# Optimization experiments

Measured on AMD Instinct MI355X. Metric: run time of the kernel, lower is better.

The kernel has to match this reference:

```python
import jax, jax.numpy as jnp
import numpy as np

D_MODEL = 1024
N_HEADS = 16
D_HEAD = D_MODEL // N_HEADS


def setup_inputs() -> dict:
    key = jax.random.key(0)
    k1, k2, k3 = jax.random.split(key, 3)
    x = jax.random.normal(k1, (2, 2048, D_MODEL), dtype=jnp.float32)
    # torch Linear weights transposed to [in, out] for x @ W
    w_qkv = jax.random.normal(k2, (D_MODEL, 3 * D_MODEL), dtype=jnp.float32) * (D_MODEL ** -0.5)
    w_proj = jax.random.normal(k3, (D_MODEL, D_MODEL), dtype=jnp.float32) * (D_MODEL ** -0.5)
    return {"x": x, "w_qkv": w_qkv, "w_proj": w_proj}


def reference(x, w_qkv, w_proj):
    B, N, D = x.shape
    qkv = x @ w_qkv                              # [B, N, 3D]
    q, k, v = jnp.split(qkv, 3, axis=-1)         # each [B, N, D]

    def split_heads(t):
        return t.reshape(B, N, N_HEADS, D_HEAD).transpose(0, 2, 1, 3)  # [B, H, N, d]

    q, k, v = map(split_heads, (q, k, v))
    scale = 1.0 / jnp.sqrt(jnp.float32(D_HEAD))
    scores = jnp.einsum('bhnd,bhmd->bhnm', q, k) * scale   # [B, H, N, N]
    attn = jax.nn.softmax(scores, axis=-1)
    out = jnp.einsum('bhnm,bhmd->bhnd', attn, v)            # [B, H, N, d]
    out = out.transpose(0, 2, 1, 3).reshape(B, N, D)        # merge heads
    return out @ w_proj + x
```

## Files before the change

### kernel.cpp

```cpp
#include <hip/hip_runtime.h>
#include <hip/hip_bf16.h>
#include <cstdint>
#include <cstddef>

typedef __bf16 bf16;
typedef __attribute__((ext_vector_type(4))) float f32x4;
typedef __attribute__((ext_vector_type(16))) float f32x16;
typedef __attribute__((ext_vector_type(8))) __bf16 bf16x8;
typedef __attribute__((ext_vector_type(4))) __bf16 bf16x4;
typedef __attribute__((ext_vector_type(4))) unsigned int u32x4;

#define D_MODEL 1024
#define NHEADS  16
#define DHEAD   64
#define SEQ     2048
#define BATCH   2
#define MROWS   (BATCH*SEQ)
#define BHTOT   (BATCH*NHEADS)

#define QSCALE 0.18033688011112042f
#define DEFER_THR 11.5f

__device__ __forceinline__ void gload16(const bf16* g, bf16* l) {
  __builtin_amdgcn_global_load_lds(
      (const __attribute__((address_space(1))) void*)g,
      (__attribute__((address_space(3))) void*)l, 16, 0, 0);
}

__device__ __forceinline__ f32x4 mfma16(bf16x8 a, bf16x8 b, f32x4 c) {
  return __builtin_amdgcn_mfma_f32_16x16x32_bf16(a, b, c, 0, 0, 0);
}

__device__ __forceinline__ f32x16 mfma32(bf16x8 a, bf16x8 b, f32x16 c) {
  return __builtin_amdgcn_mfma_f32_32x32x16_bf16(a, b, c, 0, 0, 0);
}

__device__ __forceinline__ float fexp2(float x) {
#if __has_builtin(__builtin_amdgcn_exp2f)
  return __builtin_amdgcn_exp2f(x);
#else
  float r; asm("v_exp_f32 %0, %1" : "=v"(r) : "v"(x)); return r;
#endif
}

__device__ __forceinline__ unsigned cvtpk(float lo, float hi) {
  unsigned r;
  asm("v_cvt_pk_bf16_f32 %0, %1, %2" : "=v"(r) : "v"(lo), "v"(hi));
  return r;
}


__global__ void cast_f32_bf16(const float* __restrict__ in, bf16* __restrict__ out, int n4) {
  int i = blockIdx.x * blockDim.x + threadIdx.x;
  if (i >= n4) return;
  float4 v = ((const float4*)in)[i];
  bf16x4 o;
  o[0] = (bf16)v.x; o[1] = (bf16)v.y; o[2] = (bf16)v.z; o[3] = (bf16)v.w;
  ((bf16x4*)out)[i] = o;
}

__global__ void tcast(const float* __restrict__ in, bf16* __restrict__ out, int R, int C) {
  __shared__ float t[32][33];
  int c0 = blockIdx.x * 32, r0 = blockIdx.y * 32;
  int tx = threadIdx.x, ty = threadIdx.y;
  #pragma unroll
  for (int i = 0; i < 4; i++)
    t[ty + i*8][tx] = in[(size_t)(r0 + ty + i*8) * C + c0 + tx];
  __syncthreads();
  #pragma unroll
  for (int i = 0; i < 4; i++)
    out[(size_t)(c0 + ty + i*8) * R + r0 + tx] = (bf16)t[tx][ty + i*8];
}


template <int EPI>
__global__ __launch_bounds__(256, 3) void gemm_bt(
    const bf16* __restrict__ A, const bf16* __restrict__ Bt, int K, int N,
    bf16* __restrict__ qb, bf16* __restrict__ kb, bf16* __restrict__ vtb,
    const float* __restrict__ xres, float* __restrict__ outf) {
  __shared__ alignas(16) bf16 As[128 * 64];
  __shared__ alignas(16) bf16 Bs[128 * 64];
  const int tid = threadIdx.x;
  const int wave = tid >> 6, lane = tid & 63;
  const int wr = wave >> 1, wc = wave & 1;
  const int m0 = blockIdx.y * 128, n0 = blockIdx.x * 128;
  const int srow = lane >> 3;
  const int scol = ((lane & 7) ^ srow) * 8;
  const int lr16 = lane & 15, lg = lane >> 4;
  const int rsw = (lr16 & 7) << 4;
  const int cA = (lg * 16) ^ rsw;
  const int cB = (64 + lg * 16) ^ rsw;
  const char* aP = (const char*)As + (wr*64 + lr16) * 128;
  const char* bP = (const char*)Bs + (wc*64 + lr16) * 128;

  f32x4 acc[4][4];
  #pragma unroll
  for (int m = 0; m < 4; m++)
    #pragma unroll
    for (int n = 0; n < 4; n++) acc[m][n] = (f32x4)0.0f;

  for (int k0 = 0; k0 < K; k0 += 64) {
    #pragma unroll
    for (int j = 0; j < 4; j++) {
      const int c = wave * 4 + j;
      gload16(A  + (size_t)(m0 + c*8 + srow) * K + k0 + scol, &As[c * 512]);
      gload16(Bt + (size_t)(n0 + c*8 + srow) * K + k0 + scol, &Bs[c * 512]);
    }
    __syncthreads();
    bf16x8 af[4][2], bfr[4][2];
    #pragma unroll
    for (int m = 0; m < 4; m++) {
      af[m][0] = *(const bf16x8*)(aP + m*2048 + cA);
      af[m][1] = *(const bf16x8*)(aP + m*2048 + cB);
    }
    #pragma unroll
    for (int n = 0; n < 4; n++) {
      bfr[n][0] = *(const bf16x8*)(bP + n*2048 + cA);
      bfr[n][1] = *(const bf16x8*)(bP + n*2048 + cB);
    }
    #pragma unroll
    for (int m = 0; m < 4; m++)
      #pragma unroll
      for (int n = 0; n < 4; n++) {
        acc[m][n] = mfma16(af[m][0], bfr[n][0], acc[m][n]);
        acc[m][n] = mfma16(af[m][1], bfr[n][1], acc[m][n]);
      }
    __syncthreads();
  }

  #pragma unroll
  for (int n = 0; n < 4; n++) {
    const int colg = n0 + wc*64 + n*16 + lr16;
    if (EPI == 0) {
      const int which = colg >> 10;
      const int win = colg & 1023;
      const int h = win >> 6, d = win & 63;
      #pragma unroll
      for (int m = 0; m < 4; m++) {
        const int rowg0 = m0 + wr*64 + m*16 + lg*4;
        #pragma unroll
        for (int j = 0; j < 4; j++) {
          const int rowg = rowg0 + j;
          const int b = rowg >> 11, r = rowg & 2047;
          const int bh = (b << 4) + h;
          if (which == 2) {
            vtb[((size_t)bh * DHEAD + d) * SEQ + r] = (bf16)acc[m][n][j];
          } else {
            bf16* dst = (which == 0) ? qb : kb;
            const float sc = (which == 0) ? QSCALE : 1.0f;
            dst[((size_t)bh * SEQ + r) * DHEAD + d] = (bf16)(acc[m][n][j] * sc);
          }
        }
      }
    } else {
      #pragma unroll
      for (int m = 0; m < 4; m++) {
        const int rowg0 = m0 + wr*64 + m*16 + lg*4;
        #pragma unroll
        for (int j = 0; j < 4; j++) {
          const size_t idx = (size_t)(rowg0 + j) * N + colg;
          outf[idx] = acc[m][n][j] + xres[idx];
        }
      }
    }
  }
}

__global__ __launch_bounds__(512, 2) void attn_kernel(
    const bf16* __restrict__ q, const bf16* __restrict__ k,
    const bf16* __restrict__ vt, bf16* __restrict__ o) {
  __shared__ alignas(16) char smraw[65536];
  bf16* kvb = (bf16*)smraw;
  float* mg = (float*)smraw;

  const int tid = threadIdx.x;
  const int wave = tid >> 6, lane = tid & 63;
  const int qw = wave & 3, kh2 = wave >> 2;
  const int l31 = lane & 31, hi = lane >> 5;
  const int bh = blockIdx.y;
  const int b = bh >> 4, h = bh & 15;
  const int qr = blockIdx.x * 128 + qw * 32;
  const bf16* kh = k  + (size_t)bh * SEQ * DHEAD;
  const bf16* vh = vt + (size_t)bh * DHEAD * SEQ;

  const int srow = lane >> 3;
  const int scol = ((lane & 7) ^ srow) * 8;
  const bf16* kg = kh + (size_t)(kh2 * 1024 + qw * 16 + srow) * DHEAD + scol;
  const bf16* vg = vh + (size_t)(qw * 16 + srow) * SEQ + kh2 * 1024 + scol;
  bf16* ldsK0 = kvb + kh2 * 16384 +        qw * 1024;
  bf16* ldsK1 = kvb + kh2 * 16384 + 8192 + qw * 1024;
  bf16* ldsV0 = kvb + kh2 * 16384 + 4096 +        qw * 1024;
  bf16* ldsV1 = kvb + kh2 * 16384 + 8192 + 4096 + qw * 1024;

  const bf16* qrow = q + (size_t)bh * SEQ * DHEAD + (size_t)(qr + l31) * DHEAD;
  bf16x8 qf[4];
  #pragma unroll
  for (int ks = 0; ks < 4; ks++)
    qf[ks] = *(const bf16x8*)&qrow[ks * 16 + hi * 8];

  float mr = 0.0f, lsum = 0.0f;
  f32x16 acc0 = (f32x16)0.0f, acc1 = (f32x16)0.0f;

  const int rsw = (lane & 7) << 4;
  const int rowoff = l31 * 128;
  int cofs[4];
  #pragma unroll
  for (int ks = 0; ks < 4; ks++) cofs[ks] = (ks * 32 + hi * 16) ^ rsw;
  const char* kr0 = (const char*)(kvb + kh2 * 16384) + rowoff;
  const char* kr1 = (const char*)(kvb + kh2 * 16384 + 8192) + rowoff;
  const char* vr0 = (const char*)(kvb + kh2 * 16384 + 4096) + rowoff;
  const char* vr1 = (const char*)(kvb + kh2 * 16384 + 8192 + 4096) + rowoff;

  gload16(kg, ldsK0); gload16(kg + 8 * DHEAD, ldsK0 + 512);
  gload16(vg, ldsV0); gload16(vg + 8 * SEQ,   ldsV0 + 512);
  kg += 64 * DHEAD; vg += 64;
  __syncthreads();

  const int NT = 1024 / 64;
  for (int t = 0; t < NT; ++t) {
    bf16* dK = (t & 1) ? ldsK0 : ldsK1;
    bf16* dV = (t & 1) ? ldsV0 : ldsV1;
    if (t + 1 < NT) {
      gload16(kg, dK); gload16(kg + 8 * DHEAD, dK + 512);
      gload16(vg, dV); gload16(vg + 8 * SEQ,   dV + 512);
      kg += 64 * DHEAD; vg += 64;
    }
    const char* kr = (t & 1) ? kr1 : kr0;
    const char* vr = (t & 1) ? vr1 : vr0;

    #pragma unroll
    for (int th = 0; th < 2; ++th) {
      const int toff = th * 4096;

      const float nmr = -mr;
      f32x16 s = (f32x16)nmr;
      __builtin_amdgcn_s_setprio(1);
      #pragma unroll
      for (int ks = 0; ks < 4; ks++) {
        bf16x8 kf = *(const bf16x8*)(kr + toff + cofs[ks]);
        s = mfma32(kf, qf[ks], s);
      }
      __builtin_amdgcn_s_setprio(0);

      const float a0 = fmaxf(fmaxf(s[0], s[1]), fmaxf(s[2], s[3]));
      const float a1 = fmaxf(fmaxf(s[4], s[5]), fmaxf(s[6], s[7]));
      const float a2 = fmaxf(fmaxf(s[8], s[9]), fmaxf(s[10], s[11]));
      const float a3 = fmaxf(fmaxf(s[12], s[13]), fmaxf(s[14], s[15]));
      const float lmax = fmaxf(fmaxf(a0, a1), fmaxf(a2, a3));

      if (!__all(lmax <= DEFER_THR)) {
        float mx = fmaxf(lmax, __shfl_xor(lmax, 32));
        mx = fmaxf(mx, 0.0f);
        const float corr = fexp2(-mx);
        lsum *= corr;
        acc0 *= corr; acc1 *= corr;
        mr += mx;
        #pragma unroll
        for (int r = 0; r < 16; r++) s[r] -= mx;
      }

      #pragma unroll
      for (int r = 0; r < 16; r++) s[r] = fexp2(s[r]);
      lsum += (((s[0] + s[1]) + (s[2] + s[3])) + ((s[4] + s[5]) + (s[6] + s[7])))
            + (((s[8] + s[9]) + (s[10] + s[11])) + ((s[12] + s[13]) + (s[14] + s[15])));

      __builtin_amdgcn_s_setprio(1);
      #pragma unroll
      for (int u = 0; u < 2; ++u) {
        const unsigned w0 = cvtpk(s[8*u + 0], s[8*u + 1]);
        const unsigned w1 = cvtpk(s[8*u + 2], s[8*u + 3]);
        const unsigned w2 = cvtpk(s[8*u + 4], s[8*u + 5]);
        const unsigned w3 = cvtpk(s[8*u + 6], s[8*u + 7]);
        const unsigned p0 = (unsigned)__shfl_xor((int)w0, 32);
        const unsigned p1 = (unsigned)__shfl_xor((int)w1, 32);
        const unsigned p2 = (unsigned)__shfl_xor((int)w2, 32);
        const unsigned p3 = (unsigned)__shfl_xor((int)w3, 32);
        u32x4 fw;
        fw[0] = hi ? p2 : w0;
        fw[1] = hi ? p3 : w1;
        fw[2] = hi ? w2 : p0;
        fw[3] = hi ? w3 : p1;
        bf16x8 pf = __builtin_bit_cast(bf16x8, fw);
        const int ksl = 2 * th + u;
        bf16x8 vf0 = *(const bf16x8*)(vr + cofs[ksl]);
        bf16x8 vf1 = *(const bf16x8*)(vr + 4096 + cofs[ksl]);
        acc0 = mfma32(vf0, pf, acc0);
        acc1 = mfma32(vf1, pf, acc1);
      }
      __builtin_amdgcn_s_setprio(0);
    }

    __syncthreads();
  }

  lsum += __shfl_xor(lsum, 32);

  if (kh2 == 1) {
    float* dst = &mg[(qw * 64 + lane) * 35];
    #pragma unroll
    for (int r = 0; r < 16; r++) dst[r] = acc0[r];
    #pragma unroll
    for (int r = 0; r < 16; r++) dst[16 + r] = acc1[r];
    dst[32] = lsum; dst[33] = mr;
  }
  __syncthreads();
  if (kh2 == 0) {
    const float* src = &mg[(qw * 64 + lane) * 35];
    const float lsb = src[32], mrb = src[33];
    const float M  = fmaxf(mr, mrb);
    const float wa = fexp2(mr - M), wb = fexp2(mrb - M);
    const float inv = 1.0f / (lsum * wa + lsb * wb);
    const float fa = wa * inv, fb = wb * inv;

    bf16* orow = o + ((size_t)(b * SEQ + qr + l31)) * D_MODEL + h * 64 + hi * 4;
    #pragma unroll
    for (int g = 0; g < 4; g++) {
      bf16x4 o0, o1;
      #pragma unroll
      for (int e = 0; e < 4; e++) {
        o0[e] = (bf16)(acc0[4*g + e] * fa + src[4*g + e] * fb);
        o1[e] = (bf16)(acc1[4*g + e] * fa + src[16 + 4*g + e] * fb);
      }
      *(bf16x4*)&orow[8 * g]      = o0;
      *(bf16x4*)&orow[32 + 8 * g] = o1;
    }
  }
}


extern "C" void kernel_launch(void* const* d_in, const int* in_sizes, int n_in,
                              void* d_out, int out_size, void* d_ws, size_t ws_size,
                              hipStream_t stream) {
  const float* x      = (const float*)d_in[0];
  const float* w_qkv  = (const float*)d_in[1];
  const float* w_proj = (const float*)d_in[2];
  float* outf = (float*)d_out;

  bf16* xb    = (bf16*)d_ws;
  bf16* wqkvT = xb    + (size_t)MROWS * D_MODEL;
  bf16* wpT   = wqkvT + (size_t)3 * D_MODEL * D_MODEL;
  bf16* qb    = wpT   + (size_t)D_MODEL * D_MODEL;
  bf16* kb    = qb    + (size_t)BHTOT * SEQ * DHEAD;
  bf16* vtb   = kb    + (size_t)BHTOT * SEQ * DHEAD;
  bf16* ob    = xb;

  dim3 tb(32, 8);

  cast_f32_bf16<<<(MROWS * D_MODEL / 4 + 255) / 256, 256, 0, stream>>>(
      x, xb, MROWS * D_MODEL / 4);
  tcast<<<dim3(3 * D_MODEL / 32, D_MODEL / 32), tb, 0, stream>>>(
      w_qkv, wqkvT, D_MODEL, 3 * D_MODEL);
  tcast<<<dim3(D_MODEL / 32, D_MODEL / 32), tb, 0, stream>>>(
      w_proj, wpT, D_MODEL, D_MODEL);

  gemm_bt<0><<<dim3(3 * D_MODEL / 128, MROWS / 128), 256, 0, stream>>>(
      xb, wqkvT, D_MODEL, 3 * D_MODEL, qb, kb, vtb, nullptr, nullptr);

  attn_kernel<<<dim3(SEQ / 128, BHTOT), 512, 0, stream>>>(qb, kb, vtb, ob);

  gemm_bt<1><<<dim3(D_MODEL / 128, MROWS / 128), 256, 0, stream>>>(
      ob, wpT, D_MODEL, D_MODEL, nullptr, nullptr, nullptr, x, outf);
}
```

Baseline: 134.9 us.

## Load V fragments directly from global, halve LDS, raise occupancy target

V fragments are now read straight from global memory into registers each tile instead of being staged through double-buffered LDS, which shrinks the shared allocation from 64KB to 36KB. Launch bounds are raised to request four blocks per CU. The P-fragment exchange is also trimmed from four cross-half shuffles to two. The intent is to free LDS for higher occupancy and cut LDS traffic and shuffles, at the cost of global-load latency exposed inside the loop and tighter register limits.

```diff
diff --git a/kernel.cpp b/kernel.cpp
--- a/kernel.cpp
+++ b/kernel.cpp
@@ -166,10 +166,10 @@
   }
 }
 
-__global__ __launch_bounds__(512, 2) void attn_kernel(
+__global__ __launch_bounds__(512, 4) void attn_kernel(
     const bf16* __restrict__ q, const bf16* __restrict__ k,
     const bf16* __restrict__ vt, bf16* __restrict__ o) {
-  __shared__ alignas(16) char smraw[65536];
+  __shared__ alignas(16) char smraw[36864];
   bf16* kvb = (bf16*)smraw;
   float* mg = (float*)smraw;
 
@@ -186,11 +186,11 @@
   const int srow = lane >> 3;
   const int scol = ((lane & 7) ^ srow) * 8;
   const bf16* kg = kh + (size_t)(kh2 * 1024 + qw * 16 + srow) * DHEAD + scol;
-  const bf16* vg = vh + (size_t)(qw * 16 + srow) * SEQ + kh2 * 1024 + scol;
-  bf16* ldsK0 = kvb + kh2 * 16384 +        qw * 1024;
-  bf16* ldsK1 = kvb + kh2 * 16384 + 8192 + qw * 1024;
-  bf16* ldsV0 = kvb + kh2 * 16384 + 4096 +        qw * 1024;
-  bf16* ldsV1 = kvb + kh2 * 16384 + 8192 + 4096 + qw * 1024;
+  bf16* ldsK0 = kvb + kh2 * 8192 +        qw * 1024;
+  bf16* ldsK1 = kvb + kh2 * 8192 + 4096 + qw * 1024;
+
+  const bf16* v0p = vh + (size_t)l31 * SEQ + kh2 * 1024 + hi * 8;
+  const bf16* v1p = vh + (size_t)(32 + l31) * SEQ + kh2 * 1024 + hi * 8;
 
   const bf16* qrow = q + (size_t)bh * SEQ * DHEAD + (size_t)(qr + l31) * DHEAD;
   bf16x8 qf[4];
@@ -206,27 +206,28 @@
   int cofs[4];
   #pragma unroll
   for (int ks = 0; ks < 4; ks++) cofs[ks] = (ks * 32 + hi * 16) ^ rsw;
-  const char* kr0 = (const char*)(kvb + kh2 * 16384) + rowoff;
-  const char* kr1 = (const char*)(kvb + kh2 * 16384 + 8192) + rowoff;
-  const char* vr0 = (const char*)(kvb + kh2 * 16384 + 4096) + rowoff;
-  const char* vr1 = (const char*)(kvb + kh2 * 16384 + 8192 + 4096) + rowoff;
+  const char* kr0 = (const char*)(kvb + kh2 * 8192) + rowoff;
+  const char* kr1 = (const char*)(kvb + kh2 * 8192 + 4096) + rowoff;
 
   gload16(kg, ldsK0); gload16(kg + 8 * DHEAD, ldsK0 + 512);
-  gload16(vg, ldsV0); gload16(vg + 8 * SEQ,   ldsV0 + 512);
-  kg += 64 * DHEAD; vg += 64;
+  kg += 64 * DHEAD;
   __syncthreads();
 
   const int NT = 1024 / 64;
   for (int t = 0; t < NT; ++t) {
     bf16* dK = (t & 1) ? ldsK0 : ldsK1;
-    bf16* dV = (t & 1) ? ldsV0 : ldsV1;
     if (t + 1 < NT) {
       gload16(kg, dK); gload16(kg + 8 * DHEAD, dK + 512);
-      gload16(vg, dV); gload16(vg + 8 * SEQ,   dV + 512);
-      kg += 64 * DHEAD; vg += 64;
+      kg += 64 * DHEAD;
     }
     const char* kr = (t & 1) ? kr1 : kr0;
-    const char* vr = (t & 1) ? vr1 : vr0;
+    const int kv0 = t * 64;
+
+    bf16x8 vfa0, vfa1, vfb0, vfb1, vfc0, vfc1, vfd0, vfd1;
+    vfa0 = *(const bf16x8*)(v0p + kv0);      vfa1 = *(const bf16x8*)(v1p + kv0);
+    vfb0 = *(const bf16x8*)(v0p + kv0 + 16); vfb1 = *(const bf16x8*)(v1p + kv0 + 16);
+    vfc0 = *(const bf16x8*)(v0p + kv0 + 32); vfc1 = *(const bf16x8*)(v1p + kv0 + 32);
+    vfd0 = *(const bf16x8*)(v0p + kv0 + 48); vfd1 = *(const bf16x8*)(v1p + kv0 + 48);
 
     #pragma unroll
     for (int th = 0; th < 2; ++th) {
@@ -271,19 +272,19 @@
         const unsigned w1 = cvtpk(s[8*u + 2], s[8*u + 3]);
         const unsigned w2 = cvtpk(s[8*u + 4], s[8*u + 5]);
         const unsigned w3 = cvtpk(s[8*u + 6], s[8*u + 7]);
-        const unsigned p0 = (unsigned)__shfl_xor((int)w0, 32);
-        const unsigned p1 = (unsigned)__shfl_xor((int)w1, 32);
-        const unsigned p2 = (unsigned)__shfl_xor((int)w2, 32);
-        const unsigned p3 = (unsigned)__shfl_xor((int)w3, 32);
+        const unsigned t0 = hi ? w0 : w2;
+        const unsigned t1 = hi ? w1 : w3;
+        const unsigned r0 = (unsigned)__shfl_xor((int)t0, 32);
+        const unsigned r1 = (unsigned)__shfl_xor((int)t1, 32);
         u32x4 fw;
-        fw[0] = hi ? p2 : w0;
-        fw[1] = hi ? p3 : w1;
-        fw[2] = hi ? w2 : p0;
-        fw[3] = hi ? w3 : p1;
+        fw[0] = hi ? r0 : w0;
+        fw[1] = hi ? r1 : w1;
+        fw[2] = hi ? w2 : r0;
+        fw[3] = hi ? w3 : r1;
         bf16x8 pf = __builtin_bit_cast(bf16x8, fw);
         const int ksl = 2 * th + u;
-        bf16x8 vf0 = *(const bf16x8*)(vr + cofs[ksl]);
-        bf16x8 vf1 = *(const bf16x8*)(vr + 4096 + cofs[ksl]);
+        bf16x8 vf0 = (ksl == 0) ? vfa0 : (ksl == 1) ? vfb0 : (ksl == 2) ? vfc0 : vfd0;
+        bf16x8 vf1 = (ksl == 0) ? vfa1 : (ksl == 1) ? vfb1 : (ksl == 2) ? vfc1 : vfd1;
         acc0 = mfma32(vf0, pf, acc0);
         acc1 = mfma32(vf1, pf, acc1);
       }
```

Result: slower. 192.2 us (+42.5%).
